# Performance work log

Measured on AMD Instinct MI355X. Metric: run time of the kernel, lower is better.

Reference implementation:

```python
import jax, jax.numpy as jnp
import numpy as np

H = 64          # index_n_heads
D = 128         # index_head_dim (== FP8 quant block size -> one scale per row)
RD = 64         # qk_rope_head_dim
TOPK = 512      # index_topk
THETA = 10000.0
SM_SCALE = D ** -0.5


def _fwht(x):
    """Sylvester-ordered fast Walsh-Hadamard transform over last dim, scaled by d^-0.5."""
    d = x.shape[-1]
    orig = x.shape
    y = x.reshape(-1, d)
    m = 1
    while m < d:  # static loop, log2(d)=7 iters
        y = y.reshape(-1, d // (2 * m), 2, m)
        a, b = y[:, :, 0, :], y[:, :, 1, :]
        y = jnp.stack([a + b, a - b], axis=2)
        m *= 2
    return y.reshape(orig) * (d ** -0.5)


def _interleaved_to_half(x):
    # [..., d] with (even, odd) interleaving -> [evens..., odds...]
    return jnp.concatenate([x[..., 0::2], x[..., 1::2]], axis=-1)


def _rope_half(x, cos, sin):
    # x: [..., RD] in half format; cos/sin broadcastable to [..., RD//2]
    x1, x2 = x[..., : RD // 2], x[..., RD // 2:]
    return jnp.concatenate([x1 * cos - x2 * sin, x2 * cos + x1 * sin], axis=-1)


def _layernorm(x, g, b, eps=1e-5):
    mu = jnp.mean(x, axis=-1, keepdims=True)
    var = jnp.mean(jnp.square(x - mu), axis=-1, keepdims=True)
    return (x - mu) * jax.lax.rsqrt(var + eps) * g + b


def _fp8_ue8m0_quant(x2d):
    """Per-row FP8 e4m3 quantization with UE8M0 (power-of-two) scales. x2d: (M, 128)."""
    amax = jnp.maximum(jnp.max(jnp.abs(x2d), axis=1), 1e-4)
    sf = jnp.exp2(jnp.ceil(jnp.log2(amax / 448.0)))               # (M,)
    xq = (x2d * (1.0 / sf)[:, None]).astype(jnp.float8_e4m3fn)
    return xq, sf


def _indexer_fwd(hidden_states, q_lora, positions, wq_b, wk, w_proj, ln_gamma, ln_beta):
    T = hidden_states.shape[0]
    # --- projections ---
    q = (q_lora @ wq_b).reshape(T, H, D)                          # (T,H,D)
    k = _layernorm(hidden_states @ wk, ln_gamma, ln_beta)         # (T,D)
    # --- RoPE on leading RD dims (interleaved -> half, then half rotation) ---
    inv_freq = 1.0 / (THETA ** (jnp.arange(0, RD, 2, dtype=jnp.float32) / RD))  # (RD/2,)
    ang = positions.astype(jnp.float32)[:, None] * inv_freq       # (T,RD/2)
    cos, sin = jnp.cos(ang), jnp.sin(ang)
    q_rot = _rope_half(_interleaved_to_half(q[..., :RD]), cos[:, None, :], sin[:, None, :])
    k_rot = _rope_half(_interleaved_to_half(k[..., :RD]), cos, sin)
    q = jnp.concatenate([q_rot, q[..., RD:]], axis=-1)
    k = jnp.concatenate([k_rot, k[..., RD:]], axis=-1)
    # --- Hadamard rotation ---
    q = _fwht(q)
    k = _fwht(k)
    # --- FP8 UE8M0 quantization (head_dim == quant block -> 1 scale per row) ---
    q_fp8, q_scale = _fp8_ue8m0_quant(q.reshape(T * H, D))
    k_fp8, k_scale = _fp8_ue8m0_quant(k)
    q_scale = q_scale.reshape(T, H)
    # --- gate weights: weights_proj * H^-0.5 * q_scale * softmax_scale ---
    weights = (hidden_states @ w_proj) * (H ** -0.5) * q_scale * SM_SCALE  # (T,H)
    # --- MQA indexer scoring: dequant matmul, ReLU, head-weighted sum ---
    qd = q_fp8.astype(jnp.float32).reshape(T, H, D)
    kd = k_fp8.astype(jnp.float32) * k_scale[:, None]             # (T,D)
    logits = jnp.einsum('thd,sd->ths', qd, kd)                    # (T,H,S)
    scores = jnp.einsum('th,ths->ts', weights, jax.nn.relu(logits))  # (T,S)
    # --- causal mask + top-k token selection ---
    t_idx = jnp.arange(T)
    causal = t_idx[None, :] <= t_idx[:, None]                     # (T,S): s <= t
    scores = jnp.where(causal, scores, jnp.float32(-1e30))
    vals, idx = jax.lax.top_k(scores, TOPK)
    return vals, idx


def setup_inputs() -> dict:
    key = jax.random.key(0)
    ks = jax.random.split(key, 5)
    T, HID, R = 1024, 7168, 1536
    return {
        'hidden_states': jax.random.normal(ks[0], (T, HID), jnp.float32),
        'q_lora': jax.random.normal(ks[1], (T, R), jnp.float32),
        'positions': jnp.arange(T, dtype=jnp.int32),
        'wq_b': jax.random.normal(ks[2], (R, H * D), jnp.float32) * (R ** -0.5),
        'wk': jax.random.normal(ks[3], (HID, D), jnp.float32) * (HID ** -0.5),
        'w_proj': jax.random.normal(ks[4], (HID, H), jnp.float32) * (HID ** -0.5),
        'ln_gamma': jnp.ones((D,), jnp.float32),
        'ln_beta': jnp.zeros((D,), jnp.float32),
    }


def reference(hidden_states, q_lora, positions, wq_b, wk, w_proj, ln_gamma, ln_beta):
    return _indexer_fwd(hidden_states, q_lora, positions, wq_b, wk, w_proj, ln_gamma, ln_beta)
```

## Files before the change

### kernel.cpp

```cpp
#include <hip/hip_runtime.h>
#include <cstdint>
#include <cmath>

#define NT 1024
#define NHID 7168
#define NR 1536
#define NH 64
#define ND 128
#define NTOPK 512
#define TTILE 4
#define KSPLIT 16

typedef float f32x4 __attribute__((ext_vector_type(4)));
typedef long lx2 __attribute__((ext_vector_type(2)));

__device__ __forceinline__ ushort f2bf(float x) {
  uint32_t u = __float_as_uint(x);
  u += 0x7fffu + ((u >> 16) & 1u);
  return (ushort)(u >> 16);
}
__device__ __forceinline__ float bf2f(ushort u) {
  return __uint_as_float(((uint32_t)u) << 16);
}
__device__ __forceinline__ void gload_lds16(const void* g, void* l) {
  __builtin_amdgcn_global_load_lds(
      (const __attribute__((address_space(1))) uint32_t*)g,
      (__attribute__((address_space(3))) uint32_t*)l, 16, 0, 0);
}
__device__ __forceinline__ uint32_t pk_fp8x4(float a, float b, float c, float d) {
  uint32_t lo = (uint32_t)__builtin_amdgcn_cvt_pk_fp8_f32(a, b, 0, false) & 0xffffu;
  uint32_t hi = (uint32_t)__builtin_amdgcn_cvt_pk_fp8_f32(c, d, 0, false) << 16;
  return lo | hi;
}


__device__ __forceinline__ void rope_fwht_quant(
    float v0, float v1, int l, int pos_t,
    const float* __restrict__ cost, const float* __restrict__ sint,
    uint8_t* __restrict__ out_bytes, float* __restrict__ out_scale) {
  float a = __shfl(v0, (2 * l) & 63, 64);
  float b = __shfl(v0, (2 * l + 1) & 63, 64);
  int fi = l & 31;
  float c = cost[pos_t * 32 + fi];
  float sn = sint[pos_t * 32 + fi];
  float r;
  if (l < 32)
    r = __fsub_rn(__fmul_rn(a, c), __fmul_rn(b, sn));
  else
    r = __fadd_rn(__fmul_rn(b, c), __fmul_rn(a, sn));
  v0 = r;

#pragma unroll
  for (int m = 1; m < 64; m <<= 1) {
    float p0 = __shfl_xor(v0, m, 64);
    float p1 = __shfl_xor(v1, m, 64);
    bool up = (l & m) == 0;
    v0 = up ? __fadd_rn(v0, p0) : __fsub_rn(p0, v0);
    v1 = up ? __fadd_rn(v1, p1) : __fsub_rn(p1, v1);
  }
  {
    float A0 = v0, B0 = v1;
    v0 = __fadd_rn(A0, B0);
    v1 = __fsub_rn(A0, B0);
  }
  const float WS = 0.08838834764831843f;
  v0 = __fmul_rn(v0, WS);
  v1 = __fmul_rn(v1, WS);

  float am = fmaxf(fabsf(v0), fabsf(v1));
#pragma unroll
  for (int m = 1; m < 64; m <<= 1) am = fmaxf(am, __shfl_xor(am, m, 64));
  am = fmaxf(am, 1e-4f);
  float ratio = __fdiv_rn(am, 448.0f);
  uint32_t rb = __float_as_uint(ratio);
  int e = (int)((rb + 0x7fffffu) >> 23) - 127;
  float sf = __uint_as_float((uint32_t)(e + 127) << 23);
  float inv = __uint_as_float((uint32_t)(127 - e) << 23);
  float q0 = __fmul_rn(v0, inv);
  float q1 = __fmul_rn(v1, inv);
  int b0 = __builtin_amdgcn_cvt_pk_fp8_f32(q0, q0, 0, false);
  int b1 = __builtin_amdgcn_cvt_pk_fp8_f32(q1, q1, 0, false);
  out_bytes[l] = (uint8_t)(b0 & 0xff);
  out_bytes[l + 64] = (uint8_t)(b1 & 0xff);
  if (l == 0) *out_scale = sf;
}

__global__ __launch_bounds__(256)
void prep_all_k(const float* __restrict__ hidden, const float* __restrict__ q_lora,
                const float* __restrict__ wk, const float* __restrict__ wp,
                const float* __restrict__ wq_b, const int* __restrict__ pos,
                uint32_t* __restrict__ hidden8, uint32_t* __restrict__ qlora8,
                uint8_t* __restrict__ wkp8, uint8_t* __restrict__ wqb8,
                float* __restrict__ cost, float* __restrict__ sint) {
  __shared__ uint8_t t8[64][68];
  int bid = blockIdx.x, tid = threadIdx.x;
  if (bid < 4352) {
    bool isq = bid >= 3584;
    size_t i = (size_t)(isq ? bid - 3584 : bid) * 256 + tid;
    const float* src = isq ? q_lora : hidden;
    uint32_t* dst = isq ? qlora8 : hidden8;
    const f32x4* pp = (const f32x4*)(src + i * 8);
    f32x4 a = pp[0], b = pp[1];
    size_t blk = i >> 3;
    int j = (int)(i & 7);
    size_t dw = blk * 16 + (size_t)((j & 3) * 4 + (j >> 2) * 2);
    dst[dw] = pk_fp8x4(a[0], a[1], a[2], a[3]);
    dst[dw + 1] = pk_fp8x4(b[0], b[1], b[2], b[3]);
    if (bid < NT && tid < 32) {
      int t = bid, ii = tid;
      double x = (double)(2 * ii) / 64.0;
      double pw = pow(10000.0, x);
      float p32 = (float)pw;
      float invf = __fdiv_rn(1.0f, p32);
      float ang = __fmul_rn((float)pos[t], invf);
      cost[t * 32 + ii] = (float)cos((double)ang);
      sint[t * 32 + ii] = (float)sin((double)ang);
    }
    return;
  }
  const float* in;
  uint8_t* out;
  int N_, n0, orow0, Kdim, k0;
  float scale;
  if (bid < 4688) {
    int local = bid - 4352;
    int bx = local % 3, by = local / 3;
    in = (bx < 2) ? wk : wp;
    N_ = (bx < 2) ? ND : NH;
    n0 = (bx < 2) ? bx * 64 : 0;
    orow0 = (bx < 2) ? bx * 64 : 128;
    Kdim = NHID;
    k0 = by * 64;
    out = wkp8;
    scale = 64.0f;
  } else {
    int local = bid - 4688;
    int nx = local % 128, ky = local / 128;
    in = wq_b;
    N_ = NH * ND;
    n0 = nx * 64;
    orow0 = n0;
    Kdim = NR;
    k0 = ky * 64;
    out = wqb8;
    scale = 1.0f;
  }
  int r = tid >> 4, c = (tid & 15) * 4;
#pragma unroll
  for (int rr = 0; rr < 64; rr += 16) {
    f32x4 v = *(const f32x4*)(in + (size_t)(k0 + rr + r) * N_ + n0 + c);
    *(uint32_t*)&t8[rr + r][c] =
        pk_fp8x4(v[0] * scale, v[1] * scale, v[2] * scale, v[3] * scale);
  }
  __syncthreads();
  int sp = ((c >> 3) & 3) * 16 + (c >> 5) * 8 + ((c >> 2) & 1) * 4;
#pragma unroll
  for (int rr = 0; rr < 64; rr += 16) {
    int orow = rr + r;
    uint32_t w = (uint32_t)t8[c + 0][orow] | ((uint32_t)t8[c + 1][orow] << 8) |
                 ((uint32_t)t8[c + 2][orow] << 16) | ((uint32_t)t8[c + 3][orow] << 24);
    *(uint32_t*)(out + (size_t)(orow0 + orow) * Kdim + k0 + sp) = w;
  }
}

template <int BM, int BN, bool FUSEQ>
__global__ __launch_bounds__(256)
void gemm_fp8_k(const uint8_t* __restrict__ A, const uint8_t* __restrict__ Bt,
                float* __restrict__ C, const float* __restrict__ cost,
                const float* __restrict__ sint, uint8_t* __restrict__ qfp8,
                float* __restrict__ qscale, int M, int N, int K, int kchunk) {
  constexpr int FM = BM / 32;
  constexpr int FN = BN / 32;
  constexpr int ABYTES = BM * 64;
  constexpr int BBYTES = BN * 64;
  constexpr int BUF = ABYTES + BBYTES;
  constexpr int OVER = FUSEQ ? BM * 132 * 2 : 0;
  constexpr int SMEM = (OVER > 2 * BUF) ? OVER : 2 * BUF;
  __shared__ char smem[SMEM];
  int tid = threadIdx.x;
  int wave = tid >> 6, lane = tid & 63;
  int ln = lane & 15, lg = lane >> 4;
  int n0 = blockIdx.x * BN, m0 = blockIdx.y * BM;
  int k0 = blockIdx.z * kchunk;
  int wm = (wave >> 1) * (BM / 2), wn = (wave & 1) * (BN / 2);

  f32x4 acc[FM][FN];
#pragma unroll
  for (int m = 0; m < FM; m++)
#pragma unroll
    for (int n = 0; n < FN; n++) acc[m][n] = {0.f, 0.f, 0.f, 0.f};

  auto stage = [&](int buf, int kk0) {
    char* base = smem + buf * BUF;
#pragma unroll
    for (int c = 0; c < BM / 64; c++) {
      int o = c * 256 + tid;
      int row = o >> 2, gd = o & 3;
      int gs = gd ^ ((row >> 1) & 3);
      gload_lds16(A + (size_t)(m0 + row) * K + kk0 + gs * 16, base + o * 16);
    }
#pragma unroll
    for (int c = 0; c < BN / 64; c++) {
      int o = c * 256 + tid;
      int row = o >> 2, gd = o & 3;
      int gs = gd ^ ((row >> 1) & 3);
      gload_lds16(Bt + (size_t)(n0 + row) * K + kk0 + gs * 16,
                  base + ABYTES + o * 16);
    }
  };

  int ntile = kchunk / 64;
  stage(0, k0);
  __syncthreads();
  int cur = 0;
  for (int t = 0; t < ntile; t++) {
    if (t + 1 < ntile) stage(cur ^ 1, k0 + (t + 1) * 64);
    const uint8_t* ap = (const uint8_t*)smem + cur * BUF;
    const uint8_t* bp = ap + ABYTES;
    lx2 av[FM], bv[FN];
#pragma unroll
    for (int m = 0; m < FM; m++) {
      int row = wm + m * 16 + ln;
      av[m] = *(const lx2*)(ap + row * 64 + ((lg ^ ((row >> 1) & 3)) << 4));
    }
#pragma unroll
    for (int n = 0; n < FN; n++) {
      int row = wn + n * 16 + ln;
      bv[n] = *(const lx2*)(bp + row * 64 + ((lg ^ ((row >> 1) & 3)) << 4));
    }
#pragma unroll
    for (int m = 0; m < FM; m++)
#pragma unroll
      for (int n = 0; n < FN; n++)
        acc[m][n] = __builtin_amdgcn_mfma_f32_16x16x32_fp8_fp8(
            av[m][0], bv[n][0], acc[m][n], 0, 0, 0);
#pragma unroll
    for (int m = 0; m < FM; m++)
#pragma unroll
      for (int n = 0; n < FN; n++)
        acc[m][n] = __builtin_amdgcn_mfma_f32_16x16x32_fp8_fp8(
            av[m][1], bv[n][1], acc[m][n], 0, 0, 0);
    __syncthreads();
    cur ^= 1;
  }

  if constexpr (FUSEQ) {
    ushort(*qtile)[132] = (ushort(*)[132])smem;
#pragma unroll
    for (int m = 0; m < FM; m++)
#pragma unroll
      for (int n = 0; n < FN; n++)
#pragma unroll
        for (int j = 0; j < 4; j++)
          qtile[wm + m * 16 + lg * 4 + j][wn + n * 16 + ln] = f2bf(acc[m][n][j]);
    __syncthreads();
    int h = blockIdx.x;
    for (int r = 0; r < BM / 4; r++) {
      int row = wave * (BM / 4) + r;
      int tq = m0 + row;
      float v0 = bf2f(qtile[row][lane]);
      float v1 = bf2f(qtile[row][64 + lane]);
      rope_fwht_quant(v0, v1, lane, tq, cost, sint,
                      qfp8 + ((size_t)tq * NH + h) * ND,
                      qscale + (size_t)tq * NH + h);
    }
  } else {
    float* Cz = C + (size_t)blockIdx.z * M * N;
#pragma unroll
    for (int m = 0; m < FM; m++)
#pragma unroll
      for (int n = 0; n < FN; n++)
#pragma unroll
        for (int j = 0; j < 4; j++) {
          int row = m0 + wm + m * 16 + lg * 4 + j;
          int col = n0 + wn + n * 16 + ln;
          Cz[(size_t)row * N + col] = acc[m][n][j];
        }
  }
}

__global__ __launch_bounds__(256)
void kfin_weights_k(const float* __restrict__ kpart, const float* __restrict__ gamma,
                    const float* __restrict__ beta, const float* __restrict__ cost,
                    const float* __restrict__ sint, const float* __restrict__ qscale,
                    uint8_t* __restrict__ kfp8, float* __restrict__ kscale,
                    float* __restrict__ weights) {
  int l = threadIdx.x & 63;
  int row = blockIdx.x * 4 + (threadIdx.x >> 6);
  float v0 = 0.0f, v1 = 0.0f, ws = 0.0f;
#pragma unroll
  for (int p = 0; p < KSPLIT; p++) {
    const float* base = kpart + (size_t)p * (NT * 192) + row * 192;
    v0 = __fadd_rn(v0, base[l]);
    v1 = __fadd_rn(v1, base[l + 64]);
    ws = __fadd_rn(ws, base[128 + l]);
  }
  float w = __fmul_rn(ws, 0.001953125f);
  w = __fmul_rn(w, qscale[row * NH + l]);
  w = __fmul_rn(w, 0.08838834764831843f);
  weights[row * NH + l] = w;
  float s = __fadd_rn(v0, v1);
#pragma unroll
  for (int m = 1; m < 64; m <<= 1) s = __fadd_rn(s, __shfl_xor(s, m, 64));
  float mu = __fmul_rn(s, 0.0078125f);
  float d0 = __fsub_rn(v0, mu), d1 = __fsub_rn(v1, mu);
  float vs = __fadd_rn(__fmul_rn(d0, d0), __fmul_rn(d1, d1));
#pragma unroll
  for (int m = 1; m < 64; m <<= 1) vs = __fadd_rn(vs, __shfl_xor(vs, m, 64));
  float var = __fmul_rn(vs, 0.0078125f);
  float rs = (float)(1.0 / sqrt((double)__fadd_rn(var, 1e-5f)));
  v0 = __fadd_rn(__fmul_rn(__fmul_rn(d0, rs), gamma[l]), beta[l]);
  v1 = __fadd_rn(__fmul_rn(__fmul_rn(d1, rs), gamma[l + 64]), beta[l + 64]);
  rope_fwht_quant(v0, v1, l, row, cost, sint, kfp8 + (size_t)row * ND, kscale + row);
}

__global__ __launch_bounds__(256)
void scores_k(const uint8_t* __restrict__ qfp8, const uint8_t* __restrict__ kfp8,
              const float* __restrict__ weights, float* __restrict__ scores) {
  __shared__ uint8_t q_lds[TTILE * 64 * 128];
  __shared__ uint8_t k_lds[128 * 128];
  __shared__ float w_lds[TTILE * 64];

  int b = blockIdx.x;
  int g = 0;
  while (g < 7 && b >= 16 * (g + 1) * (g + 2)) g++;
  int r = b - 16 * g * (g + 1);
  int a = 32 * g + r / (g + 1);
  int chunk = r % (g + 1);
  int t0 = a * TTILE;
  int s0 = chunk * 128;

  int tid = threadIdx.x;
  int wave = tid >> 6, lane = tid & 63;
  int lg = lane >> 4, ln = lane & 15;

  const uint8_t* qbase = qfp8 + (size_t)t0 * 64 * 128;
#pragma unroll
  for (int it = 0; it < 8; it++) {
    int o = it * 256 + wave * 64 + lane;
    int row = o >> 3, G = o & 7;
    int src = row * 128 + ((G ^ ((row >> 1) & 7)) << 4);
    gload_lds16(qbase + src, q_lds + (it * 256 + wave * 64) * 16);
  }
  const uint8_t* kbase = kfp8 + (size_t)s0 * 128;
#pragma unroll
  for (int it = 0; it < 4; it++) {
    int o = it * 256 + wave * 64 + lane;
    int row = o >> 3, G = o & 7;
    int src = row * 128 + ((G ^ ((row >> 1) & 7)) << 4);
    gload_lds16(kbase + src, k_lds + (it * 256 + wave * 64) * 16);
  }
  w_lds[tid] = weights[t0 * NH + tid];
  __syncthreads();

  long bfr[2][4];
#pragma unroll
  for (int sj = 0; sj < 2; sj++) {
    int srow = wave * 32 + sj * 16 + ln;
    int base = srow * 128;
    int xr = ((srow >> 1) & 7) << 4;
#pragma unroll
    for (int ks = 0; ks < 4; ks++)
      bfr[sj][ks] = *(const long*)(k_lds + base + ((ks * 32 + lg * 8) ^ xr));
  }

  float p[TTILE][2];
#pragma unroll
  for (int tt = 0; tt < TTILE; tt++) p[tt][0] = p[tt][1] = 0.0f;

#pragma unroll
  for (int ht = 0; ht < 4; ht++) {
    long afr[TTILE][4];
#pragma unroll
    for (int tt = 0; tt < TTILE; tt++) {
      int qrow = tt * 64 + ht * 16 + ln;
      int base = qrow * 128;
      int xr = ((qrow >> 1) & 7) << 4;
#pragma unroll
      for (int ks = 0; ks < 4; ks++)
        afr[tt][ks] = *(const long*)(q_lds + base + ((ks * 32 + lg * 8) ^ xr));
    }
#pragma unroll
    for (int tt = 0; tt < TTILE; tt++) {
      float wj[4];
#pragma unroll
      for (int j = 0; j < 4; j++) wj[j] = w_lds[tt * 64 + ht * 16 + lg * 4 + j];
#pragma unroll
      for (int sj = 0; sj < 2; sj++) {
        f32x4 acc = {0.f, 0.f, 0.f, 0.f};
#pragma unroll
        for (int ks = 0; ks < 4; ks++)
          acc = __builtin_amdgcn_mfma_f32_16x16x32_fp8_fp8(afr[tt][ks], bfr[sj][ks],
                                                           acc, 0, 0, 0);
#pragma unroll
        for (int j = 0; j < 4; j++)
          p[tt][sj] = fmaf(wj[j], fmaxf(acc[j], 0.0f), p[tt][sj]);
      }
    }
  }

#pragma unroll
  for (int tt = 0; tt < TTILE; tt++)
#pragma unroll
    for (int sj = 0; sj < 2; sj++) {
      float v = p[tt][sj];
      v += __shfl_xor(v, 16, 64);
      v += __shfl_xor(v, 32, 64);
      if (lg == 0)
        scores[(size_t)(t0 + tt) * NT + s0 + wave * 32 + sj * 16 + ln] = v;
    }
}

__global__ __launch_bounds__(256)
void topk_k(const float* __restrict__ scores, const float* __restrict__ kscale,
            float* __restrict__ outv, float* __restrict__ outi) {
  __shared__ unsigned long long key[1024];
  int t = blockIdx.x, tid = threadIdx.x;
#pragma unroll
  for (int p = 0; p < 4; p++) {
    int s = tid + p * 256;
    float v;
    if (s <= t) {
      v = __fmul_rn(scores[(size_t)t * NT + s], kscale[s]);
    } else {
      v = -1e30f;
    }
    unsigned u = __float_as_uint(v);
    unsigned ou = (u & 0x80000000u) ? ~u : (u | 0x80000000u);
    key[s] = ((unsigned long long)ou << 32) | (unsigned)(~(unsigned)s);
  }
  for (int k = 2; k <= 1024; k <<= 1) {
    for (int j = k >> 1; j > 0; j >>= 1) {
      __syncthreads();
#pragma unroll
      for (int p = 0; p < 2; p++) {
        int i = tid + p * 256;
        int l = ((i & ~(j - 1)) << 1) | (i & (j - 1));
        int m = l + j;
        bool desc = ((l & k) == 0);
        unsigned long long a = key[l], b = key[m];
        if (desc ? (a < b) : (a > b)) {
          key[l] = b;
          key[m] = a;
        }
      }
    }
  }
  __syncthreads();
#pragma unroll
  for (int p = 0; p < 2; p++) {
    int r = tid + p * 256;
    unsigned long long kk = key[r];
    unsigned ou = (unsigned)(kk >> 32);
    unsigned u = (ou & 0x80000000u) ? (ou ^ 0x80000000u) : ~ou;
    unsigned idx = (~(unsigned)(kk & 0xffffffffu)) & 1023u;
    outv[(size_t)t * NTOPK + r] = __uint_as_float(u);
    outi[(size_t)t * NTOPK + r] = (float)idx;
  }
}

extern "C" void kernel_launch(void* const* d_in, const int* in_sizes, int n_in,
                              void* d_out, int out_size, void* d_ws, size_t ws_size,
                              hipStream_t stream) {
  const float* hidden = (const float*)d_in[0];
  const float* q_lora = (const float*)d_in[1];
  const int* positions = (const int*)d_in[2];
  const float* wq_b = (const float*)d_in[3];
  const float* wk = (const float*)d_in[4];
  const float* w_proj = (const float*)d_in[5];
  const float* ln_g = (const float*)d_in[6];
  const float* ln_b = (const float*)d_in[7];
  float* out = (float*)d_out;

  char* u0 = (char*)d_ws;
  uint8_t* hidden8 = (uint8_t*)u0;
  uint8_t* wkp8 = (uint8_t*)(u0 + 7340032);
  uint8_t* wqb8 = (uint8_t*)(u0 + 8716288);
  uint8_t* qlora8 = (uint8_t*)(u0 + 21299200);
  float* scores = (float*)u0;
  char* p = u0 + 22872064;
  float* kpart = (float*)p;    p += 12582912;
  float* cost = (float*)p;     p += 131072;
  float* sint = (float*)p;     p += 131072;
  float* kscale = (float*)p;   p += 4096;
  float* qscale = (float*)p;   p += 262144;
  float* weights = (float*)p;  p += 262144;
  uint8_t* kfp8 = (uint8_t*)p; p += 131072;
  uint8_t* qfp8 = (uint8_t*)p; p += 8388608;

  prep_all_k<<<7760, 256, 0, stream>>>(hidden, q_lora, wk, w_proj, wq_b,
                                       positions, (uint32_t*)hidden8,
                                       (uint32_t*)qlora8, wkp8, wqb8,
                                       cost, sint);

  gemm_fp8_k<64, 64, false><<<dim3(3, 16, KSPLIT), 256, 0, stream>>>(
      hidden8, wkp8, kpart, nullptr, nullptr, nullptr, nullptr,
      NT, 192, NHID, NHID / KSPLIT);

  gemm_fp8_k<64, 128, true><<<dim3(64, 16, 1), 256, 0, stream>>>(
      qlora8, wqb8, nullptr, cost, sint, qfp8, qscale,
      NT, NH * ND, NR, NR);

  kfin_weights_k<<<NT / 4, 256, 0, stream>>>(kpart, ln_g, ln_b, cost, sint,
                                             qscale, kfp8, kscale, weights);

  scores_k<<<1152, 256, 0, stream>>>(qfp8, kfp8, weights, scores);
  topk_k<<<NT, 256, 0, stream>>>(scores, kscale, out, out + (size_t)NT * NTOPK);
}
```

Before: 114.5 us.

## Merge K and Q FP8 GEMMs into one launch and halve K split

Folds the two FP8 GEMM kernels (the split-K hidden×wk/w_proj GEMM and the fused Q GEMM with RoPE/FWHT/quant) into one kernel that dispatches by block index. The two workloads now share the GPU concurrently instead of running back to back, and one launch is removed. KSPLIT drops from 16 to 8, giving fewer, longer K-blocks, half the partial-sum buffer and less reduction work in kfin. The risk is that the longer K-blocks become a tail behind the Q blocks, and that the shared LDS size is fixed for the larger of the two configs.

```diff
diff --git a/kernel.cpp b/kernel.cpp
--- a/kernel.cpp
+++ b/kernel.cpp
@@ -9,7 +9,7 @@
 #define ND 128
 #define NTOPK 512
 #define TTILE 4
-#define KSPLIT 16
+#define KSPLIT 8
 
 typedef float f32x4 __attribute__((ext_vector_type(4)));
 typedef long lx2 __attribute__((ext_vector_type(2)));
@@ -164,24 +164,22 @@
 }
 
 template <int BM, int BN, bool FUSEQ>
-__global__ __launch_bounds__(256)
-void gemm_fp8_k(const uint8_t* __restrict__ A, const uint8_t* __restrict__ Bt,
-                float* __restrict__ C, const float* __restrict__ cost,
-                const float* __restrict__ sint, uint8_t* __restrict__ qfp8,
-                float* __restrict__ qscale, int M, int N, int K, int kchunk) {
+__device__ __forceinline__
+void gemm_body(char* smem, const uint8_t* __restrict__ A,
+               const uint8_t* __restrict__ Bt, float* __restrict__ C,
+               const float* __restrict__ cost, const float* __restrict__ sint,
+               uint8_t* __restrict__ qfp8, float* __restrict__ qscale,
+               int M, int N, int K, int kchunk, int bx, int by, int bz) {
   constexpr int FM = BM / 32;
   constexpr int FN = BN / 32;
   constexpr int ABYTES = BM * 64;
   constexpr int BBYTES = BN * 64;
   constexpr int BUF = ABYTES + BBYTES;
-  constexpr int OVER = FUSEQ ? BM * 132 * 2 : 0;
-  constexpr int SMEM = (OVER > 2 * BUF) ? OVER : 2 * BUF;
-  __shared__ char smem[SMEM];
   int tid = threadIdx.x;
   int wave = tid >> 6, lane = tid & 63;
   int ln = lane & 15, lg = lane >> 4;
-  int n0 = blockIdx.x * BN, m0 = blockIdx.y * BM;
-  int k0 = blockIdx.z * kchunk;
+  int n0 = bx * BN, m0 = by * BM;
+  int k0 = bz * kchunk;
   int wm = (wave >> 1) * (BM / 2), wn = (wave & 1) * (BN / 2);
 
   f32x4 acc[FM][FN];
@@ -254,7 +252,7 @@
         for (int j = 0; j < 4; j++)
           qtile[wm + m * 16 + lg * 4 + j][wn + n * 16 + ln] = f2bf(acc[m][n][j]);
     __syncthreads();
-    int h = blockIdx.x;
+    int h = bx;
     for (int r = 0; r < BM / 4; r++) {
       int row = wave * (BM / 4) + r;
       int tq = m0 + row;
@@ -265,7 +263,7 @@
                       qscale + (size_t)tq * NH + h);
     }
   } else {
-    float* Cz = C + (size_t)blockIdx.z * M * N;
+    float* Cz = C + (size_t)bz * M * N;
 #pragma unroll
     for (int m = 0; m < FM; m++)
 #pragma unroll
@@ -276,6 +274,26 @@
           int col = n0 + wn + n * 16 + ln;
           Cz[(size_t)row * N + col] = acc[m][n][j];
         }
+  }
+}
+
+__global__ __launch_bounds__(256)
+void gemm_all_k(const uint8_t* __restrict__ qlora8, const uint8_t* __restrict__ wqb8,
+                const uint8_t* __restrict__ hidden8, const uint8_t* __restrict__ wkp8,
+                float* __restrict__ kpart, const float* __restrict__ cost,
+                const float* __restrict__ sint, uint8_t* __restrict__ qfp8,
+                float* __restrict__ qscale) {
+  __shared__ char smem[24576];
+  int bid = blockIdx.x;
+  if (bid < 1024) {
+    gemm_body<64, 128, true>(smem, qlora8, wqb8, nullptr, cost, sint, qfp8,
+                             qscale, NT, NH * ND, NR, NR,
+                             bid & 63, bid >> 6, 0);
+  } else {
+    int kb = bid - 1024;
+    gemm_body<64, 64, false>(smem, hidden8, wkp8, kpart, nullptr, nullptr,
+                             nullptr, nullptr, NT, 192, NHID, NHID / KSPLIT,
+                             kb % 3, (kb / 3) & 15, kb / 48);
   }
 }
 
@@ -479,7 +497,7 @@
   uint8_t* qlora8 = (uint8_t*)(u0 + 21299200);
   float* scores = (float*)u0;
   char* p = u0 + 22872064;
-  float* kpart = (float*)p;    p += 12582912;
+  float* kpart = (float*)p;    p += 6291456;
   float* cost = (float*)p;     p += 131072;
   float* sint = (float*)p;     p += 131072;
   float* kscale = (float*)p;   p += 4096;
@@ -493,13 +511,8 @@
                                        (uint32_t*)qlora8, wkp8, wqb8,
                                        cost, sint);
 
-  gemm_fp8_k<64, 64, false><<<dim3(3, 16, KSPLIT), 256, 0, stream>>>(
-      hidden8, wkp8, kpart, nullptr, nullptr, nullptr, nullptr,
-      NT, 192, NHID, NHID / KSPLIT);
-
-  gemm_fp8_k<64, 128, true><<<dim3(64, 16, 1), 256, 0, stream>>>(
-      qlora8, wqb8, nullptr, cost, sint, qfp8, qscale,
-      NT, NH * ND, NR, NR);
+  gemm_all_k<<<1408, 256, 0, stream>>>(qlora8, wqb8, hidden8, wkp8, kpart,
+                                       cost, sint, qfp8, qscale);
 
   kfin_weights_k<<<NT / 4, 256, 0, stream>>>(kpart, ln_g, ln_b, cost, sint,
                                              qscale, kfp8, kscale, weights);
```

After: 107.4 us (median of 2 runs). 6.2% less time.
